# Performance work log

Hardware: AMD Instinct MI355X
Metric: run time of the kernel (lower is better)

## Reference

```python
import jax, jax.numpy as jnp
import numpy as np

DIM = 1024
HEADS = 16
DIM_HEAD = 64
INNER = HEADS * DIM_HEAD
THETA = 10000.0
EPS = 1e-5


def setup_inputs() -> dict:
    key = jax.random.key(0)
    k1, k2, k3, k4 = jax.random.split(key, 4)
    b, n = 4, 2048
    x = jax.random.normal(k1, (b, n, DIM), dtype=jnp.float32)
    gamma = jnp.ones((DIM,), jnp.float32)
    beta = jnp.zeros((DIM,), jnp.float32)
    w_qkv = jax.random.normal(k2, (DIM, 3 * INNER), dtype=jnp.float32) * (DIM ** -0.5)
    w_out = jax.random.normal(k3, (INNER, DIM), dtype=jnp.float32) * (INNER ** -0.5)
    b_out = jax.random.normal(k4, (DIM,), dtype=jnp.float32) * 0.01
    return {"x": x, "gamma": gamma, "beta": beta, "w_qkv": w_qkv, "w_out": w_out, "b_out": b_out}


def _rope_cos_sin(n, d, dtype):
    # freqs_cis = exp(i * t * theta^{-2j/d}) for j in [0, d/2)
    inv = 1.0 / (THETA ** (jnp.arange(0, d, 2, dtype=jnp.float32) / d))  # (d/2,)
    ang = jnp.arange(n, dtype=jnp.float32)[:, None] * inv[None, :]       # (n, d/2)
    return jnp.cos(ang).astype(dtype), jnp.sin(ang).astype(dtype)


def _apply_rope(t, cos, sin):
    # t: (b, n, h, d); rotate adjacent pairs along d
    b, n, h, d = t.shape
    tr = t.reshape(b, n, h, d // 2, 2)
    e, o = tr[..., 0], tr[..., 1]
    c = cos[None, :, None, :]
    s = sin[None, :, None, :]
    out = jnp.stack([e * c - o * s, e * s + o * c], axis=-1)
    return out.reshape(b, n, h, d)


def reference(x, gamma, beta, w_qkv, w_out, b_out):
    b, n, _ = x.shape
    # LayerNorm
    mu = jnp.mean(x, axis=-1, keepdims=True)
    var = jnp.mean(jnp.square(x - mu), axis=-1, keepdims=True)
    xn = (x - mu) * jax.lax.rsqrt(var + EPS) * gamma + beta
    # QKV projection (no bias)
    qkv = xn @ w_qkv  # (b, n, 3*INNER)
    q, k, v = jnp.split(qkv, 3, axis=-1)
    q = q.reshape(b, n, HEADS, DIM_HEAD)
    k = k.reshape(b, n, HEADS, DIM_HEAD)
    v = v.reshape(b, n, HEADS, DIM_HEAD)
    # RoPE on q, k (per head, global_start_pos = 0)
    cos, sin = _rope_cos_sin(n, DIM_HEAD, x.dtype)
    q = _apply_rope(q, cos, sin)
    k = _apply_rope(k, cos, sin)
    # attention
    scale = DIM_HEAD ** -0.5
    dots = jnp.einsum('bnhd,bmhd->bhnm', q, k) * scale
    attn = jax.nn.softmax(dots, axis=-1)
    out = jnp.einsum('bhnm,bmhd->bnhd', attn, v).reshape(b, n, INNER)
    return out @ w_out + b_out
```

## Files before the change

kernel.cpp:

```cpp
#include <hip/hip_runtime.h>
#include <hip/hip_fp16.h>

typedef __attribute__((ext_vector_type(8))) short short8;
typedef __attribute__((ext_vector_type(4))) short short4v;
typedef __attribute__((ext_vector_type(4))) float floatx4;
typedef _Float16 half8 __attribute__((ext_vector_type(8)));
typedef __fp16 fp16x2 __attribute__((ext_vector_type(2)));
typedef __attribute__((ext_vector_type(4))) unsigned uintx4;

extern "C" __device__ float __ocml_native_exp2_f32(float);

static __device__ __forceinline__ short f2h(float f) {
    _Float16 h = (_Float16)f;
    return __builtin_bit_cast(short, h);
}

static __device__ __forceinline__ unsigned pkrtz(float a, float b) {
    fp16x2 h = __builtin_amdgcn_cvt_pkrtz(a, b);
    return __builtin_bit_cast(unsigned, h);
}

static __device__ __forceinline__ void drain_all() { __builtin_amdgcn_s_waitcnt(0); }

static __device__ __forceinline__ floatx4 mfma16(short8 a, short8 b, floatx4 c) {
    return __builtin_amdgcn_mfma_f32_16x16x32_f16(__builtin_bit_cast(half8, a),
                                                  __builtin_bit_cast(half8, b), c, 0, 0, 0);
}

static __device__ __forceinline__ void async16(const void* g, void* l) {
    __builtin_amdgcn_global_load_lds((const __attribute__((address_space(1))) void*)g,
                                     (__attribute__((address_space(3))) void*)l, 16, 0, 0);
}

__global__ __launch_bounds__(256) void ln_kernel(const float* __restrict__ x,
                                                 const float* __restrict__ gamma,
                                                 const float* __restrict__ beta,
                                                 short* __restrict__ xh) {
    __shared__ float red[8];
    const int row = blockIdx.x, tid = threadIdx.x;
    const int w = tid >> 6, lane = tid & 63;
    const float4 v = ((const float4*)(x + (size_t)row * 1024))[tid];
    float s = v.x + v.y + v.z + v.w;
    float ss = v.x * v.x + v.y * v.y + v.z * v.z + v.w * v.w;
#pragma unroll
    for (int off = 32; off; off >>= 1) {
        s += __shfl_xor(s, off);
        ss += __shfl_xor(ss, off);
    }
    if (lane == 0) { red[w] = s; red[4 + w] = ss; }
    __syncthreads();
    s = red[0] + red[1] + red[2] + red[3];
    ss = red[4] + red[5] + red[6] + red[7];
    const float mu = s * (1.f / 1024.f);
    const float rs = rsqrtf(ss * (1.f / 1024.f) - mu * mu + 1e-5f);
    const float4 g = ((const float4*)gamma)[tid];
    const float4 bt = ((const float4*)beta)[tid];
    short4v ph;
    ph[0] = f2h((v.x - mu) * rs * g.x + bt.x);
    ph[1] = f2h((v.y - mu) * rs * g.y + bt.y);
    ph[2] = f2h((v.z - mu) * rs * g.z + bt.z);
    ph[3] = f2h((v.w - mu) * rs * g.w + bt.w);
    *(short4v*)(xh + (size_t)row * 1024 + tid * 4) = ph;
}

__global__ void tcast_h(const float* __restrict__ in, short* __restrict__ out, int R, int C) {
    __shared__ float t[32][33];
    const int bx = blockIdx.x * 32, by = blockIdx.y * 32;
    const int tx = threadIdx.x, ty = threadIdx.y;
#pragma unroll
    for (int i = 0; i < 32; i += 8) t[ty + i][tx] = in[(size_t)(by + ty + i) * C + bx + tx];
    __syncthreads();
#pragma unroll
    for (int i = 0; i < 32; i += 8) out[(size_t)(bx + ty + i) * R + by + tx] = f2h(t[tx][ty + i]);
}

__global__ __launch_bounds__(256, 2) void gemm_qkv(const short* __restrict__ A,
                                                   const short* __restrict__ BT,
                                                   short* __restrict__ Qd, short* __restrict__ Kd,
                                                   short* __restrict__ VTb) {
    extern __shared__ __align__(16) short pool[];
    short* sA = pool;
    short* sB = pool + 4096;
    short* sOut = pool;

    const int tid = threadIdx.x;
    const int w = tid >> 6, lane = tid & 63, quad = lane >> 4, l15 = lane & 15;
    const int wm = w >> 1, wn = w & 1;
    const int m0 = blockIdx.y * 128, n0 = blockIdx.x * 128;
    const int qsw = (quad ^ ((l15 >> 1) & 3)) * 8;

    floatx4 acc[4][4];
#pragma unroll
    for (int i = 0; i < 4; i++)
#pragma unroll
        for (int j = 0; j < 4; j++) acc[i][j] = (floatx4){0.f, 0.f, 0.f, 0.f};

    for (int k0 = 0; k0 < 1024; k0 += 32) {
        drain_all();
        __syncthreads();
#pragma unroll
        for (int i = 0; i < 2; ++i) {
            int c = i * 256 + tid;
            int r = c >> 2, kc = ((c & 3) ^ ((r >> 1) & 3)) << 3;
            async16(A + (size_t)(m0 + r) * 1024 + k0 + kc, (char*)sA + c * 16);
            async16(BT + (size_t)(n0 + r) * 1024 + k0 + kc, (char*)sB + c * 16);
        }
        drain_all();
        __syncthreads();
        short8 af[4], bf[4];
#pragma unroll
        for (int t = 0; t < 4; t++) {
            af[t] = *(const short8*)(sA + (wm * 64 + t * 16 + l15) * 32 + qsw);
            bf[t] = *(const short8*)(sB + (wn * 64 + t * 16 + l15) * 32 + qsw);
        }
#pragma unroll
        for (int tm = 0; tm < 4; tm++)
#pragma unroll
            for (int tn = 0; tn < 4; tn++) acc[tm][tn] = mfma16(af[tm], bf[tn], acc[tm][tn]);
    }

    drain_all();
    __syncthreads();

    const int b = m0 >> 11, nnb = m0 & 2047;
    const bool isV = (n0 >= 2048);
    if (!isV) {
        const float qs = (n0 < 1024) ? 0.18033688011112042f : 1.0f;
#pragma unroll
        for (int tn = 0; tn < 4; tn++) {
            const int d = tn * 16 + l15;
            const int colL = wn * 64 + tn * 16 + l15;
            const float inv = exp2f((float)(d >> 1) * -0.4152410118609203f);
#pragma unroll
            for (int tm = 0; tm < 4; tm++) {
                const int rowL = wm * 64 + tm * 16 + quad * 4;
#pragma unroll
                for (int i = 0; i < 4; i++) {
                    float v = acc[tm][tn][i];
                    float pv = __shfl_xor(v, 1);
                    float ang = (float)(nnb + rowL + i) * inv;
                    float sn = __sinf(ang), cs = __cosf(ang);
                    float r = (d & 1) ? (pv * sn + v * cs) : (v * cs - pv * sn);
                    sOut[(rowL + i) * 136 + colL] = f2h(r * qs);
                }
            }
        }
        __syncthreads();
        short* dst0 = (n0 < 1024) ? Qd : Kd;
        const int hbase = (n0 & 1023) >> 6;
#pragma unroll
        for (int it = 0; it < 8; ++it) {
            int c = it * 256 + tid;
            int r = c >> 4, cg = (c & 15) * 8;
            int h = hbase + (cg >> 6), d = cg & 63;
            *(short8*)(dst0 + ((size_t)((b * 16 + h) * 2048 + nnb + r)) * 64 + d) =
                *(const short8*)(sOut + r * 136 + cg);
        }
    } else {
#pragma unroll
        for (int tn = 0; tn < 4; tn++) {
            const int colL = wn * 64 + tn * 16 + l15;
#pragma unroll
            for (int tm = 0; tm < 4; tm++) {
                const int rowL = wm * 64 + tm * 16 + quad * 4;
#pragma unroll
                for (int i = 0; i < 4; i++)
                    sOut[colL * 136 + rowL + i] = f2h(acc[tm][tn][i]);
            }
        }
        __syncthreads();
        const int hbase = (n0 & 1023) >> 6;
#pragma unroll
        for (int it = 0; it < 8; ++it) {
            int c = it * 256 + tid;
            int ci = c >> 4, rg = (c & 15) * 8;
            int h = hbase + (ci >> 6), d = ci & 63;
            short8 v = *(const short8*)(sOut + ci * 136 + rg);
            if (d & 8) v = __builtin_shufflevector(v, v, 4, 5, 6, 7, 0, 1, 2, 3);
            *(short8*)(VTb + ((size_t)((b * 16 + h) * 64 + d)) * 2048 + nnb + rg) = v;
        }
    }
}

__global__ __launch_bounds__(256, 2) void gemm_out(const short* __restrict__ A,
                                                   const short* __restrict__ BT,
                                                   float* __restrict__ Fout,
                                                   const float* __restrict__ bias) {
    __shared__ __align__(16) short sA[128 * 32];
    __shared__ __align__(16) short sB[128 * 32];
    const int tid = threadIdx.x;
    const int w = tid >> 6, lane = tid & 63, quad = lane >> 4, l15 = lane & 15;
    const int wm = w >> 1, wn = w & 1;
    const int m0 = blockIdx.y * 128, n0 = blockIdx.x * 128;
    const int qsw = (quad ^ ((l15 >> 1) & 3)) * 8;

    floatx4 acc[4][4];
#pragma unroll
    for (int i = 0; i < 4; i++)
#pragma unroll
        for (int j = 0; j < 4; j++) acc[i][j] = (floatx4){0.f, 0.f, 0.f, 0.f};

    for (int k0 = 0; k0 < 1024; k0 += 32) {
        drain_all();
        __syncthreads();
#pragma unroll
        for (int i = 0; i < 2; ++i) {
            int c = i * 256 + tid;
            int r = c >> 2, kc = ((c & 3) ^ ((r >> 1) & 3)) << 3;
            async16(A + (size_t)(m0 + r) * 1024 + k0 + kc, (char*)sA + c * 16);
            async16(BT + (size_t)(n0 + r) * 1024 + k0 + kc, (char*)sB + c * 16);
        }
        drain_all();
        __syncthreads();
        short8 af[4], bf[4];
#pragma unroll
        for (int t = 0; t < 4; t++) af[t] = *(const short8*)(sA + (wm * 64 + t * 16 + l15) * 32 + qsw);
#pragma unroll
        for (int t = 0; t < 4; t++) bf[t] = *(const short8*)(sB + (wn * 64 + t * 16 + l15) * 32 + qsw);
#pragma unroll
        for (int tm = 0; tm < 4; tm++)
#pragma unroll
            for (int tn = 0; tn < 4; tn++) acc[tm][tn] = mfma16(af[tm], bf[tn], acc[tm][tn]);
    }

#pragma unroll
    for (int tn = 0; tn < 4; tn++) {
        const int col = n0 + wn * 64 + tn * 16 + l15;
        const float bb = bias[col];
#pragma unroll
        for (int tm = 0; tm < 4; tm++) {
            const int row0 = m0 + wm * 64 + tm * 16 + quad * 4;
#pragma unroll
            for (int i = 0; i < 4; i++) Fout[(size_t)(row0 + i) * 1024 + col] = acc[tm][tn][i] + bb;
        }
    }
}

__global__ __launch_bounds__(512, 4) void attn_kernel(const short* __restrict__ Qg,
                                                      const short* __restrict__ Kg,
                                                      const short* __restrict__ VTg,
                                                      short* __restrict__ Og) {
    extern __shared__ __align__(16) short apool[];
    short* sKV0 = apool;
    short* sKV1 = apool + 8192;

    const int tid = threadIdx.x;
    const int w = tid >> 6, lane = tid & 63, quad = lane >> 4, l15 = lane & 15;
    const int qt = blockIdx.x, bh = blockIdx.y;

    const short* Qp = Qg + (size_t)(bh * 2048 + qt * 256) * 64;
    const short* Kp = Kg + (size_t)bh * 2048 * 64;
    const short* Vp = VTg + (size_t)bh * 64 * 2048;

    const int str = tid >> 3, stc = tid & 7;
    const int scl = stc ^ (str & 7);
    const int kSrcOff = str * 64 + scl * 8;
    const int vSrcOff = str * 2048 + scl * 8;
    const int dstOff = tid * 16;

    short8 aq[2][2];
#pragma unroll
    for (int rb = 0; rb < 2; rb++)
#pragma unroll
        for (int kh = 0; kh < 2; kh++)
            aq[rb][kh] = *(const short8*)(Qp + (w * 32 + rb * 16 + l15) * 64 + kh * 32 + quad * 8);

    short8 ones;
#pragma unroll
    for (int j = 0; j < 8; j++) ones[j] = 0x3C00;

    floatx4 o4[2][4], ol[2];
#pragma unroll
    for (int rb = 0; rb < 2; rb++) {
#pragma unroll
        for (int dt = 0; dt < 4; dt++) o4[rb][dt] = (floatx4){0.f, 0.f, 0.f, 0.f};
        ol[rb] = (floatx4){0.f, 0.f, 0.f, 0.f};
    }

    async16(Kp + kSrcOff, (char*)sKV0 + dstOff);
    async16(Vp + vSrcOff, (char*)(sKV0 + 4096) + dstOff);

    const int swz0 = (quad ^ (l15 & 7)) << 3;
    const int swz1 = ((4 | quad) ^ (l15 & 7)) << 3;

    for (int kt = 0; kt < 32; ++kt) {
        const short* sK = (kt & 1) ? sKV1 : sKV0;
        const short* sVT = sK + 4096;
        drain_all();
        __syncthreads();
        if (kt + 1 < 32) {
            short* nK = (kt & 1) ? sKV0 : sKV1;
            const int n0 = (kt + 1) * 64;
            async16(Kp + (size_t)n0 * 64 + kSrcOff, (char*)nK + dstOff);
            async16(Vp + n0 + vSrcOff, (char*)(nK + 4096) + dstOff);
        }

#pragma unroll
        for (int nc = 0; nc < 2; nc++) {
            floatx4 zA[2], zB[2];
            {
                const int rbase = ((2 * nc) * 16 + l15) * 64;
                short8 k0 = *(const short8*)(sK + rbase + swz0);
                short8 k1 = *(const short8*)(sK + rbase + swz1);
                __builtin_amdgcn_s_setprio(1);
#pragma unroll
                for (int rb = 0; rb < 2; rb++) {
                    floatx4 z = (floatx4){0.f, 0.f, 0.f, 0.f};
                    z = mfma16(k0, aq[rb][0], z);
                    z = mfma16(k1, aq[rb][1], z);
                    zA[rb] = z;
                }
                __builtin_amdgcn_s_setprio(0);
            }
            {
                const int rbase = ((2 * nc + 1) * 16 + l15) * 64;
                short8 k0 = *(const short8*)(sK + rbase + swz0);
                short8 k1 = *(const short8*)(sK + rbase + swz1);
                __builtin_amdgcn_s_setprio(1);
#pragma unroll
                for (int rb = 0; rb < 2; rb++) {
                    floatx4 z = (floatx4){0.f, 0.f, 0.f, 0.f};
                    z = mfma16(k0, aq[rb][0], z);
                    z = mfma16(k1, aq[rb][1], z);
                    zB[rb] = z;
                }
                __builtin_amdgcn_s_setprio(0);
            }

            short8 pa[4];
            const int r7 = l15 & 7;
            const int h4 = ((quad ^ (l15 >> 3)) & 1) << 2;
            const int cLo = (((nc << 2) | (quad >> 1)) ^ r7) << 3;
            const int cHi = ((((nc << 2) + 2) | (quad >> 1)) ^ r7) << 3;
#pragma unroll
            for (int dt = 0; dt < 4; dt++) {
                const short* rowp = sVT + (dt * 16 + l15) * 64;
                short4v lo = *(const short4v*)(rowp + cLo + h4);
                short4v hi = *(const short4v*)(rowp + cHi + h4);
                pa[dt] = __builtin_shufflevector(lo, hi, 0, 1, 2, 3, 4, 5, 6, 7);
            }

#pragma unroll
            for (int rb = 0; rb < 2; rb++) {
                uintx4 pbw;
                pbw.x = pkrtz(__ocml_native_exp2_f32(zA[rb][0]),
                              __ocml_native_exp2_f32(zA[rb][1]));
                pbw.y = pkrtz(__ocml_native_exp2_f32(zA[rb][2]),
                              __ocml_native_exp2_f32(zA[rb][3]));
                pbw.z = pkrtz(__ocml_native_exp2_f32(zB[rb][0]),
                              __ocml_native_exp2_f32(zB[rb][1]));
                pbw.w = pkrtz(__ocml_native_exp2_f32(zB[rb][2]),
                              __ocml_native_exp2_f32(zB[rb][3]));
                short8 pb = __builtin_bit_cast(short8, pbw);
                __builtin_amdgcn_s_setprio(1);
#pragma unroll
                for (int dt = 0; dt < 4; dt++) o4[rb][dt] = mfma16(pa[dt], pb, o4[rb][dt]);
                ol[rb] = mfma16(ones, pb, ol[rb]);
                __builtin_amdgcn_s_setprio(0);
            }
        }
    }

    float linv[2];
    linv[0] = 1.0f / ol[0][0];
    linv[1] = 1.0f / ol[1][0];

    drain_all();
    __syncthreads();
    short* sO = apool;
#pragma unroll
    for (int rb = 0; rb < 2; rb++) {
        const int q = w * 32 + rb * 16 + l15;
#pragma unroll
        for (int dt = 0; dt < 4; dt++) {
            short4v pk;
#pragma unroll
            for (int i = 0; i < 4; i++) pk[i] = f2h(o4[rb][dt][i] * linv[rb]);
            const int d0 = dt * 16 + quad * 4;
            *(short4v*)(sO + q * 64 + (((d0 >> 3) ^ (q & 7)) << 3) + (d0 & 7)) = pk;
        }
    }
    drain_all();
    __syncthreads();
    const int b = bh >> 4, h = bh & 15;
#pragma unroll
    for (int it = 0; it < 4; ++it) {
        int g = it * 512 + tid;
        int r = g >> 3, c = g & 7;
        *(short8*)(Og + (size_t)(b * 2048 + qt * 256 + r) * 1024 + h * 64 + c * 8) =
            *(const short8*)(sO + r * 64 + ((c ^ (r & 7)) << 3));
    }
}

extern "C" void kernel_launch(void* const* d_in, const int* in_sizes, int n_in, void* d_out,
                              int out_size, void* d_ws, size_t ws_size, hipStream_t stream) {
    const float* x = (const float*)d_in[0];
    const float* gamma = (const float*)d_in[1];
    const float* beta = (const float*)d_in[2];
    const float* w_qkv = (const float*)d_in[3];
    const float* w_out = (const float*)d_in[4];
    const float* b_out = (const float*)d_in[5];
    float* out = (float*)d_out;

    char* ws = (char*)d_ws;
    short* xh = (short*)ws;
    short* wqkvT = (short*)(ws + 16777216);
    short* woT = (short*)(ws + 23068672);
    short* VTb = (short*)(ws + 25165824);
    short* Qd = (short*)d_out;
    short* Kd = (short*)d_out + 8388608;

    ln_kernel<<<8192, 256, 0, stream>>>(x, gamma, beta, xh);
    tcast_h<<<dim3(96, 32), dim3(32, 8), 0, stream>>>(w_qkv, wqkvT, 1024, 3072);
    tcast_h<<<dim3(32, 32), dim3(32, 8), 0, stream>>>(w_out, woT, 1024, 1024);
    gemm_qkv<<<dim3(24, 64), 256, 34816, stream>>>(xh, wqkvT, Qd, Kd, VTb);
    attn_kernel<<<dim3(8, 64), 512, 32768, stream>>>(Qd, Kd, VTb, xh);
    gemm_out<<<dim3(8, 64), 256, 0, stream>>>(xh, woT, out, b_out);
}
```

Measured before the change: 286.4 us.

## Double-buffer LDS tiles in QKV and output GEMMs to overlap loads with MFMA

Both projection GEMMs now use two LDS stages. The next K-tile is fetched asynchronously while MFMAs run on the current tile, which cuts the per-iteration synchronisation from two barriers to one. The launch-bounds occupancy hint is raised from 2 to 4 blocks. This doubles LDS per block, so actual occupancy may be limited by shared memory, and the higher occupancy target may constrain registers. The dynamic shared memory size for gemm_qkv must also be at least 32 KB at launch, which this code does not show.

```diff
diff --git a/kernel.cpp b/kernel.cpp
--- a/kernel.cpp
+++ b/kernel.cpp
@@ -74,13 +74,11 @@
     for (int i = 0; i < 32; i += 8) out[(size_t)(bx + ty + i) * R + by + tx] = f2h(t[tx][ty + i]);
 }
 
-__global__ __launch_bounds__(256, 2) void gemm_qkv(const short* __restrict__ A,
+__global__ __launch_bounds__(256, 4) void gemm_qkv(const short* __restrict__ A,
                                                    const short* __restrict__ BT,
                                                    short* __restrict__ Qd, short* __restrict__ Kd,
                                                    short* __restrict__ VTb) {
     extern __shared__ __align__(16) short pool[];
-    short* sA = pool;
-    short* sB = pool + 4096;
     short* sOut = pool;
 
     const int tid = threadIdx.x;
@@ -89,38 +87,55 @@
     const int m0 = blockIdx.y * 128, n0 = blockIdx.x * 128;
     const int qsw = (quad ^ ((l15 >> 1) & 3)) * 8;
 
+    int sr[2], skc[2];
+#pragma unroll
+    for (int i = 0; i < 2; ++i) {
+        int c = i * 256 + tid;
+        sr[i] = c >> 2;
+        skc[i] = ((c & 3) ^ ((sr[i] >> 1) & 3)) << 3;
+    }
+
     floatx4 acc[4][4];
 #pragma unroll
     for (int i = 0; i < 4; i++)
 #pragma unroll
         for (int j = 0; j < 4; j++) acc[i][j] = (floatx4){0.f, 0.f, 0.f, 0.f};
 
-    for (int k0 = 0; k0 < 1024; k0 += 32) {
+#pragma unroll
+    for (int i = 0; i < 2; ++i) {
+        int c = i * 256 + tid;
+        async16(A + (size_t)(m0 + sr[i]) * 1024 + skc[i], (char*)pool + c * 16);
+        async16(BT + (size_t)(n0 + sr[i]) * 1024 + skc[i], (char*)(pool + 4096) + c * 16);
+    }
+    drain_all();
+    __syncthreads();
+
+    for (int kt = 0; kt < 32; ++kt) {
+        const short* cA = pool + (kt & 1) * 8192;
+        const short* cB = cA + 4096;
+        if (kt + 1 < 32) {
+            short* nA = pool + ((kt + 1) & 1) * 8192;
+            const int k0 = (kt + 1) * 32;
+#pragma unroll
+            for (int i = 0; i < 2; ++i) {
+                int c = i * 256 + tid;
+                async16(A + (size_t)(m0 + sr[i]) * 1024 + k0 + skc[i], (char*)nA + c * 16);
+                async16(BT + (size_t)(n0 + sr[i]) * 1024 + k0 + skc[i], (char*)(nA + 4096) + c * 16);
+            }
+        }
+        short8 af[4], bf[4];
+#pragma unroll
+        for (int t = 0; t < 4; t++) {
+            af[t] = *(const short8*)(cA + (wm * 64 + t * 16 + l15) * 32 + qsw);
+            bf[t] = *(const short8*)(cB + (wn * 64 + t * 16 + l15) * 32 + qsw);
+        }
+#pragma unroll
+        for (int tm = 0; tm < 4; tm++)
+#pragma unroll
+            for (int tn = 0; tn < 4; tn++) acc[tm][tn] = mfma16(af[tm], bf[tn], acc[tm][tn]);
         drain_all();
         __syncthreads();
-#pragma unroll
-        for (int i = 0; i < 2; ++i) {
-            int c = i * 256 + tid;
-            int r = c >> 2, kc = ((c & 3) ^ ((r >> 1) & 3)) << 3;
-            async16(A + (size_t)(m0 + r) * 1024 + k0 + kc, (char*)sA + c * 16);
-            async16(BT + (size_t)(n0 + r) * 1024 + k0 + kc, (char*)sB + c * 16);
-        }
-        drain_all();
-        __syncthreads();
-        short8 af[4], bf[4];
-#pragma unroll
-        for (int t = 0; t < 4; t++) {
-            af[t] = *(const short8*)(sA + (wm * 64 + t * 16 + l15) * 32 + qsw);
-            bf[t] = *(const short8*)(sB + (wn * 64 + t * 16 + l15) * 32 + qsw);
-        }
-#pragma unroll
-        for (int tm = 0; tm < 4; tm++)
-#pragma unroll
-            for (int tn = 0; tn < 4; tn++) acc[tm][tn] = mfma16(af[tm], bf[tn], acc[tm][tn]);
-    }
-
-    drain_all();
-    __syncthreads();
+    }
 
     const int b = m0 >> 11, nnb = m0 & 2047;
     const bool isV = (n0 >= 2048);
@@ -182,45 +197,64 @@
     }
 }
 
-__global__ __launch_bounds__(256, 2) void gemm_out(const short* __restrict__ A,
+__global__ __launch_bounds__(256, 4) void gemm_out(const short* __restrict__ A,
                                                    const short* __restrict__ BT,
                                                    float* __restrict__ Fout,
                                                    const float* __restrict__ bias) {
-    __shared__ __align__(16) short sA[128 * 32];
-    __shared__ __align__(16) short sB[128 * 32];
+    __shared__ __align__(16) short pool2[16384];
     const int tid = threadIdx.x;
     const int w = tid >> 6, lane = tid & 63, quad = lane >> 4, l15 = lane & 15;
     const int wm = w >> 1, wn = w & 1;
     const int m0 = blockIdx.y * 128, n0 = blockIdx.x * 128;
     const int qsw = (quad ^ ((l15 >> 1) & 3)) * 8;
 
+    int sr[2], skc[2];
+#pragma unroll
+    for (int i = 0; i < 2; ++i) {
+        int c = i * 256 + tid;
+        sr[i] = c >> 2;
+        skc[i] = ((c & 3) ^ ((sr[i] >> 1) & 3)) << 3;
+    }
+
     floatx4 acc[4][4];
 #pragma unroll
     for (int i = 0; i < 4; i++)
 #pragma unroll
         for (int j = 0; j < 4; j++) acc[i][j] = (floatx4){0.f, 0.f, 0.f, 0.f};
 
-    for (int k0 = 0; k0 < 1024; k0 += 32) {
+#pragma unroll
+    for (int i = 0; i < 2; ++i) {
+        int c = i * 256 + tid;
+        async16(A + (size_t)(m0 + sr[i]) * 1024 + skc[i], (char*)pool2 + c * 16);
+        async16(BT + (size_t)(n0 + sr[i]) * 1024 + skc[i], (char*)(pool2 + 4096) + c * 16);
+    }
+    drain_all();
+    __syncthreads();
+
+    for (int kt = 0; kt < 32; ++kt) {
+        const short* cA = pool2 + (kt & 1) * 8192;
+        const short* cB = cA + 4096;
+        if (kt + 1 < 32) {
+            short* nA = pool2 + ((kt + 1) & 1) * 8192;
+            const int k0 = (kt + 1) * 32;
+#pragma unroll
+            for (int i = 0; i < 2; ++i) {
+                int c = i * 256 + tid;
+                async16(A + (size_t)(m0 + sr[i]) * 1024 + k0 + skc[i], (char*)nA + c * 16);
+                async16(BT + (size_t)(n0 + sr[i]) * 1024 + k0 + skc[i], (char*)(nA + 4096) + c * 16);
+            }
+        }
+        short8 af[4], bf[4];
+#pragma unroll
+        for (int t = 0; t < 4; t++) af[t] = *(const short8*)(cA + (wm * 64 + t * 16 + l15) * 32 + qsw);
+#pragma unroll
+        for (int t = 0; t < 4; t++) bf[t] = *(const short8*)(cB + (wn * 64 + t * 16 + l15) * 32 + qsw);
+#pragma unroll
+        for (int tm = 0; tm < 4; tm++)
+#pragma unroll
+            for (int tn = 0; tn < 4; tn++) acc[tm][tn] = mfma16(af[tm], bf[tn], acc[tm][tn]);
         drain_all();
         __syncthreads();
-#pragma unroll
-        for (int i = 0; i < 2; ++i) {
-            int c = i * 256 + tid;
-            int r = c >> 2, kc = ((c & 3) ^ ((r >> 1) & 3)) << 3;
-            async16(A + (size_t)(m0 + r) * 1024 + k0 + kc, (char*)sA + c * 16);
-            async16(BT + (size_t)(n0 + r) * 1024 + k0 + kc, (char*)sB + c * 16);
-        }
-        drain_all();
-        __syncthreads();
-        short8 af[4], bf[4];
-#pragma unroll
-        for (int t = 0; t < 4; t++) af[t] = *(const short8*)(sA + (wm * 64 + t * 16 + l15) * 32 + qsw);
-#pragma unroll
-        for (int t = 0; t < 4; t++) bf[t] = *(const short8*)(sB + (wn * 64 + t * 16 + l15) * 32 + qsw);
-#pragma unroll
-        for (int tm = 0; tm < 4; tm++)
-#pragma unroll
-            for (int tn = 0; tn < 4; tn++) acc[tm][tn] = mfma16(af[tm], bf[tn], acc[tm][tn]);
     }
 
 #pragma unroll
```

Result: faster. 266.3 us (-7.0%).
